# Kernel optimization log

Hardware: AMD Instinct MI355X
Metric: run time of the kernel (lower is better)

The kernel has to match this reference:

```python
import jax, jax.numpy as jnp
import numpy as np

B, N, D = 4, 2048, 512
H, DH = 8, 64  # heads, dim_head; hidden = H*DH = 512


def setup_inputs() -> dict:
    key = jax.random.key(0)
    k1, k2, k3, k4 = jax.random.split(key, 4)
    x = jax.random.normal(k1, (B, N, D), dtype=jnp.float32)
    pos_bias = jax.random.normal(k2, (H, N, N), dtype=jnp.float32) * 0.02
    w_qkv = jax.random.normal(k3, (D, 3 * H * DH), dtype=jnp.float32) * 0.02
    w_out = jax.random.normal(k4, (H * DH, D), dtype=jnp.float32) * 0.02
    return {"x": x, "pos_bias": pos_bias, "w_qkv": w_qkv, "w_out": w_out}


def reference(x, pos_bias, w_qkv, w_out):
    scale = DH ** (-0.5)
    qkv = x @ w_qkv                                   # [B, N, 3*H*DH]
    q, k, v = jnp.split(qkv, 3, axis=-1)
    # '... n (h d) -> ... h n d'
    def split_heads(t):
        return t.reshape(B, N, H, DH).transpose(0, 2, 1, 3)  # [B, H, N, DH]
    q, k, v = split_heads(q), split_heads(k), split_heads(v)
    q = q * scale
    sim = jnp.einsum('bhid,bhjd->bhij', q, k)         # [B, H, N, N]
    sim = sim + pos_bias                              # broadcast over batch
    # original subtracts detached row-max then softmax; jax.nn.softmax does
    # the same stable (stop-gradient max-subtract) computation.
    attn = jax.nn.softmax(sim, axis=-1)
    out = jnp.einsum('bhij,bhjd->bhid', attn, v)      # [B, H, N, DH]
    out = out.transpose(0, 2, 1, 3).reshape(B, N, H * DH)
    return out @ w_out                                # [B, N, D]
```

## Files before the change

### kernel.cpp

```cpp
#include <hip/hip_runtime.h>

typedef short bf16x8 __attribute__((ext_vector_type(8)));
typedef float f32x4 __attribute__((ext_vector_type(4)));

#define MFMA16(a, b, c) __builtin_amdgcn_mfma_f32_16x16x32_bf16(a, b, c, 0, 0, 0)

__device__ __forceinline__ short f2bf(float f) {
  unsigned u = __builtin_bit_cast(unsigned, f);
  u += 0x7fffu + ((u >> 16) & 1u);
  return (short)(u >> 16);
}

__device__ __forceinline__ void gload16(const void* g, void* l) {
  __builtin_amdgcn_global_load_lds(
      (const __attribute__((address_space(1))) void*)g,
      (__attribute__((address_space(3))) void*)l, 16, 0, 0);
}

#define L2E 1.44269504088896f


__global__ __launch_bounds__(256) void cvt_bf16(const float* __restrict__ in,
                                                short* __restrict__ out) {
  size_t i = ((size_t)blockIdx.x * 256 + threadIdx.x) * 8;
  const float4* p = (const float4*)(in + i);
  float4 a = p[0], b = p[1];
  bf16x8 v;
  v[0] = f2bf(a.x); v[1] = f2bf(a.y); v[2] = f2bf(a.z); v[3] = f2bf(a.w);
  v[4] = f2bf(b.x); v[5] = f2bf(b.y); v[6] = f2bf(b.z); v[7] = f2bf(b.w);
  *(bf16x8*)(out + i) = v;
}

__global__ __launch_bounds__(256) void transpose_cvt(const float* __restrict__ in,
                                                     short* __restrict__ out,
                                                     int K, int N) {
  __shared__ short Ts[64][72];
  const int t = threadIdx.x;
  const int k0 = blockIdx.y * 64, n1 = blockIdx.x * 64;
  const int kk = t >> 2, nq = (t & 3) * 16;
  const float* src = in + (size_t)(k0 + kk) * N + n1 + nq;
#pragma unroll
  for (int i = 0; i < 16; ++i) Ts[nq + i][kk] = f2bf(src[i]);
  __syncthreads();
  const int n = t >> 2, kq = (t & 3) * 16;
  short* dst = out + (size_t)(n1 + n) * K + k0 + kq;
  *(bf16x8*)dst = *(const bf16x8*)&Ts[n][kq];
  *(bf16x8*)(dst + 8) = *(const bf16x8*)&Ts[n][kq + 8];
}


__device__ __forceinline__ void gemm128_mainloop(const short* __restrict__ A,
                                                 const short* __restrict__ BT,
                                                 int m0, int n0,
                                                 short (*As)[40], short (*Bs)[40],
                                                 f32x4 acc[4][4]) {
  const int t = threadIdx.x;
  const int w = t >> 6, lane = t & 63, l15 = lane & 15, quad = lane >> 4;
  const int wm = (w & 1) * 64, wn = (w >> 1) * 64;
  const int srow = t >> 1, skg = (t & 1) * 16;
  const short* aptr = A + (size_t)(m0 + srow) * 512 + skg;
  const short* bptr = BT + (size_t)(n0 + srow) * 512 + skg;
  for (int k0 = 0; k0 < 512; k0 += 32) {
    __syncthreads();
    *(bf16x8*)&As[srow][skg]     = *(const bf16x8*)(aptr + k0);
    *(bf16x8*)&As[srow][skg + 8] = *(const bf16x8*)(aptr + k0 + 8);
    *(bf16x8*)&Bs[srow][skg]     = *(const bf16x8*)(bptr + k0);
    *(bf16x8*)&Bs[srow][skg + 8] = *(const bf16x8*)(bptr + k0 + 8);
    __syncthreads();
    bf16x8 af[4], bfr[4];
#pragma unroll
    for (int i = 0; i < 4; ++i) af[i] = *(const bf16x8*)&As[wm + i * 16 + l15][quad * 8];
#pragma unroll
    for (int j = 0; j < 4; ++j) bfr[j] = *(const bf16x8*)&Bs[wn + j * 16 + l15][quad * 8];
#pragma unroll
    for (int i = 0; i < 4; ++i)
#pragma unroll
      for (int j = 0; j < 4; ++j)
        acc[i][j] = MFMA16(af[i], bfr[j], acc[i][j]);
  }
}


__global__ __launch_bounds__(256) void gemm_qkv(const short* __restrict__ A,
                                                const short* __restrict__ BT,
                                                short* __restrict__ q_ws,
                                                short* __restrict__ k_ws,
                                                short* __restrict__ v_t) {
  __shared__ short As[128][40];
  __shared__ short Bs[128][40];
  __shared__ short Ts[64][136];
  const int t = threadIdx.x;
  const int w = t >> 6, lane = t & 63, l15 = lane & 15, quad = lane >> 4;
  const int wm = (w & 1) * 64, wn = (w >> 1) * 64;
  const int m0 = blockIdx.y * 128, n0 = blockIdx.x * 128;
  f32x4 acc[4][4];
#pragma unroll
  for (int i = 0; i < 4; ++i)
#pragma unroll
    for (int j = 0; j < 4; ++j) acc[i][j] = (f32x4){0.f, 0.f, 0.f, 0.f};

  gemm128_mainloop(A, BT, m0, n0, As, Bs, acc);

  const int which = n0 >> 9;
  const int b = m0 >> 11, seq0 = m0 & 2047;
  if (which < 2) {
    short* dst = (which == 0) ? q_ws : k_ws;
    const float scale = (which == 0) ? (0.125f * L2E) : 1.0f;
#pragma unroll
    for (int i = 0; i < 4; ++i)
#pragma unroll
      for (int j = 0; j < 4; ++j)
#pragma unroll
        for (int r = 0; r < 4; ++r) {
          int m_loc = wm + i * 16 + quad * 4 + r;
          int col = n0 + wn + j * 16 + l15;
          int h = (col >> 6) & 7, d = col & 63;
          dst[((size_t)(b * 8 + h) * 2048 + seq0 + m_loc) * 64 + d] =
              f2bf(acc[i][j][r] * scale);
        }
  } else {
    for (int half = 0; half < 2; ++half) {
      __syncthreads();
      if ((w >> 1) == half) {
#pragma unroll
        for (int i = 0; i < 4; ++i)
#pragma unroll
          for (int j = 0; j < 4; ++j)
#pragma unroll
            for (int r = 0; r < 4; ++r)
              Ts[j * 16 + l15][wm + i * 16 + quad * 4 + r] = f2bf(acc[i][j][r]);
      }
      __syncthreads();
      const int hd = ((n0 + half * 64) >> 6) & 7;
      const int dp = t >> 2, sq = (t & 3) * 32;
      short* dstp = v_t + ((size_t)(b * 8 + hd) * 64 + dp) * 2048 + seq0 + sq;
#pragma unroll
      for (int u = 0; u < 4; ++u)
        *(bf16x8*)(dstp + u * 8) = *(const bf16x8*)&Ts[dp][sq + u * 8];
    }
  }
}


#define ATTN_STAGE(BUFD, J0N)                                                  \
  do {                                                                         \
    _Pragma("unroll") for (int i_ = 0; i_ < 2; ++i_) {                         \
      const int ch_ = w * 2 + i_;                                              \
      const int off_ = ch_ * 1024 + lane * 16;                                 \
      const int row_ = off_ >> 7;                                              \
      const int col_ = (off_ & 127) ^ ((row_ & 7) << 4);                       \
      const char* gk_ = (const char*)k_ws +                                    \
          ((size_t)bh * 2048 + (size_t)(J0N) + row_) * 128 + col_;             \
      const char* gv_ = (const char*)v_t +                                     \
          ((size_t)bh * 64 + row_) * 4096 + (size_t)(J0N) * 2 + col_;          \
      gload16(gk_, (char*)&Ks[BUFD][0][0] + ch_ * 1024);                       \
      gload16(gv_, (char*)&Vs[BUFD][0][0] + ch_ * 1024);                       \
    }                                                                          \
  } while (0)

#define ATTN_LOADB(BV, J0N)                                                    \
  do {                                                                         \
    _Pragma("unroll") for (int nt_ = 0; nt_ < 4; ++nt_)                        \
        _Pragma("unroll") for (int r_ = 0; r_ < 4; ++r_)                       \
            BV[nt_][r_] = brow[r_][(J0N) + nt_ * 16];                          \
  } while (0)

#define ATTN_BODY(BUFC, BVC, BVN, J0N, DONEXT)                                 \
  do {                                                                         \
    if (DONEXT) {                                                              \
      ATTN_STAGE((BUFC) ^ 1, (J0N));                                           \
      ATTN_LOADB(BVN, (J0N));                                                  \
    }                                                                          \
    f32x4 S_[4];                                                               \
    _Pragma("unroll") for (int nt_ = 0; nt_ < 4; ++nt_) {                      \
      const char* kb_ = (const char*)&Ks[BUFC][0][0] + (nt_ * 16 + l15) * 128; \
      bf16x8 k0_ = *(const bf16x8*)(kb_ + cs);                                 \
      bf16x8 k1_ = *(const bf16x8*)(kb_ + (cs ^ 64));                          \
      f32x4 s_ = (f32x4){0.f, 0.f, 0.f, 0.f};                                  \
      s_ = MFMA16(aQ0, k0_, s_);                                               \
      s_ = MFMA16(aQ1, k1_, s_);                                               \
      S_[nt_] = s_;                                                            \
    }                                                                          \
    _Pragma("unroll") for (int nt_ = 0; nt_ < 4; ++nt_) {                      \
      float p0_ = exp2f(fmaf(BVC[nt_][0], L2E, S_[nt_][0]));                   \
      float p1_ = exp2f(fmaf(BVC[nt_][1], L2E, S_[nt_][1]));                   \
      float p2_ = exp2f(fmaf(BVC[nt_][2], L2E, S_[nt_][2]));                   \
      float p3_ = exp2f(fmaf(BVC[nt_][3], L2E, S_[nt_][3]));                   \
      lsum[0] += p0_; lsum[1] += p1_; lsum[2] += p2_; lsum[3] += p3_;          \
      unsigned pk01_, pk23_;                                                   \
      asm("v_cvt_pk_bf16_f32 %0, %1, %2" : "=v"(pk01_) : "v"(p0_), "v"(p1_)); \
      asm("v_cvt_pk_bf16_f32 %0, %1, %2" : "=v"(pk23_) : "v"(p2_), "v"(p3_)); \
      char* pb_ = (char*)&Pw[w][0][0];                                         \
      const int c0_ = 2 * (nt_ * 16 + l15);                                    \
      const int q4_ = quad * 4;                                                \
      *(short*)(pb_ + (q4_ + 0) * 128 + (c0_ ^ (((q4_ + 0) & 7) << 4))) =      \
          (short)pk01_;                                                        \
      *(short*)(pb_ + (q4_ + 1) * 128 + (c0_ ^ (((q4_ + 1) & 7) << 4))) =      \
          (short)(pk01_ >> 16);                                                \
      *(short*)(pb_ + (q4_ + 2) * 128 + (c0_ ^ (((q4_ + 2) & 7) << 4))) =      \
          (short)pk23_;                                                        \
      *(short*)(pb_ + (q4_ + 3) * 128 + (c0_ ^ (((q4_ + 3) & 7) << 4))) =      \
          (short)(pk23_ >> 16);                                                \
    }                                                                          \
    {                                                                          \
      const char* pr_ = (const char*)&Pw[w][0][0] + l15 * 128;                 \
      bf16x8 aP0 = *(const bf16x8*)(pr_ + cs);                                 \
      bf16x8 aP1 = *(const bf16x8*)(pr_ + (cs ^ 64));                          \
      _Pragma("unroll") for (int dt_ = 0; dt_ < 4; ++dt_) {                    \
        const char* vb_ =                                                      \
            (const char*)&Vs[BUFC][0][0] + (dt_ * 16 + l15) * 128;             \
        bf16x8 v0_ = *(const bf16x8*)(vb_ + cs);                               \
        bf16x8 v1_ = *(const bf16x8*)(vb_ + (cs ^ 64));                        \
        O[dt_] = MFMA16(aP0, v0_, O[dt_]);                                     \
        O[dt_] = MFMA16(aP1, v1_, O[dt_]);                                     \
      }                                                                        \
    }                                                                          \
    __syncthreads();                                                           \
  } while (0)

__global__ __launch_bounds__(256, 4) void attn_kernel(const short* __restrict__ q_ws,
                                                      const short* __restrict__ k_ws,
                                                      const short* __restrict__ v_t,
                                                      const float* __restrict__ bias,
                                                      short* __restrict__ attnO) {
  __shared__ short Ks[2][64][64];
  __shared__ short Vs[2][64][64];
  __shared__ short Pw[4][16][64];
  const int t = threadIdx.x;
  const int w = t >> 6, lane = t & 63, l15 = lane & 15, quad = lane >> 4;
  const int bid = blockIdx.x;
  const int h = bid & 7;
  const int b = (bid >> 3) & 3;
  const int qb = bid >> 5;
  const int bh = b * 8 + h;
  const int q0 = qb * 64 + w * 16;
  const int cs = (quad * 16) ^ ((l15 & 7) << 4);

  const size_t qbase = ((size_t)bh * 2048 + q0 + l15) * 64 + quad * 8;
  bf16x8 aQ0 = *(const bf16x8*)(q_ws + qbase);
  bf16x8 aQ1 = *(const bf16x8*)(q_ws + qbase + 32);

  f32x4 O[4];
#pragma unroll
  for (int i = 0; i < 4; ++i) O[i] = (f32x4){0.f, 0.f, 0.f, 0.f};
  float lsum[4] = {0.f, 0.f, 0.f, 0.f};

  const float* brow[4];
#pragma unroll
  for (int r = 0; r < 4; ++r)
    brow[r] = bias + ((size_t)h * 2048 + q0 + quad * 4 + r) * 2048 + l15;

  float bvA[4][4], bvB[4][4];
  ATTN_STAGE(0, 0);
  ATTN_LOADB(bvA, 0);
  __syncthreads();

  for (int it = 0; it < 16; ++it) {
    const int j0 = it * 128;
    ATTN_BODY(0, bvA, bvB, j0 + 64, 1);
    ATTN_BODY(1, bvB, bvA, j0 + 128, (it < 15));
  }

#pragma unroll
  for (int off = 1; off <= 8; off <<= 1)
#pragma unroll
    for (int r = 0; r < 4; ++r) lsum[r] += __shfl_xor(lsum[r], off);
#pragma unroll
  for (int r = 0; r < 4; ++r) lsum[r] = 1.f / lsum[r];
#pragma unroll
  for (int dt = 0; dt < 4; ++dt)
#pragma unroll
    for (int r = 0; r < 4; ++r) {
      size_t row = (size_t)b * 2048 + q0 + quad * 4 + r;
      attnO[row * 512 + h * 64 + dt * 16 + l15] = f2bf(O[dt][r] * lsum[r]);
    }
#undef ATTN_STAGE
#undef ATTN_LOADB
#undef ATTN_BODY
}


__global__ __launch_bounds__(256) void gemm_out(const short* __restrict__ A,
                                                const short* __restrict__ BT,
                                                float* __restrict__ out) {
  __shared__ short As[128][40];
  __shared__ short Bs[128][40];
  const int t = threadIdx.x;
  const int w = t >> 6, lane = t & 63, l15 = lane & 15, quad = lane >> 4;
  const int wm = (w & 1) * 64, wn = (w >> 1) * 64;
  const int m0 = blockIdx.y * 128, n0 = blockIdx.x * 128;
  f32x4 acc[4][4];
#pragma unroll
  for (int i = 0; i < 4; ++i)
#pragma unroll
    for (int j = 0; j < 4; ++j) acc[i][j] = (f32x4){0.f, 0.f, 0.f, 0.f};

  gemm128_mainloop(A, BT, m0, n0, As, Bs, acc);

#pragma unroll
  for (int i = 0; i < 4; ++i)
#pragma unroll
    for (int j = 0; j < 4; ++j)
#pragma unroll
      for (int r = 0; r < 4; ++r)
        out[(size_t)(m0 + wm + i * 16 + quad * 4 + r) * 512 + n0 + wn + j * 16 + l15] =
            acc[i][j][r];
}


extern "C" void kernel_launch(void* const* d_in, const int* in_sizes, int n_in,
                              void* d_out, int out_size, void* d_ws, size_t ws_size,
                              hipStream_t stream) {
  (void)in_sizes; (void)n_in; (void)out_size; (void)ws_size;
  const float* x        = (const float*)d_in[0];
  const float* pos_bias = (const float*)d_in[1];
  const float* w_qkv    = (const float*)d_in[2];
  const float* w_out    = (const float*)d_in[3];
  float* out = (float*)d_out;

  short* ws = (short*)d_ws;
  const size_t SEG = (size_t)32 * 2048 * 64;
  short* q_ws  = ws;
  short* k_ws  = q_ws + SEG;
  short* v_t   = k_ws + SEG;
  short* attnO = v_t + SEG;
  short* xbf   = attnO + SEG;
  short* wqkvT = xbf + SEG;
  short* woutT = wqkvT + (size_t)1536 * 512;

  cvt_bf16<<<2048, 256, 0, stream>>>(x, xbf);
  transpose_cvt<<<dim3(24, 8), 256, 0, stream>>>(w_qkv, wqkvT, 512, 1536);
  transpose_cvt<<<dim3(8, 8), 256, 0, stream>>>(w_out, woutT, 512, 512);
  gemm_qkv<<<dim3(12, 64), 256, 0, stream>>>(xbf, wqkvT, q_ws, k_ws, v_t);
  attn_kernel<<<1024, 256, 0, stream>>>(q_ws, k_ws, v_t, pos_bias, attnO);
  gemm_out<<<dim3(4, 64), 256, 0, stream>>>(attnO, woutT, out);
}
```

Before: 374.5 us.

## Double-buffer GEMM mainloop with async global-to-LDS loads and XOR swizzle

Replaces the synchronous register-staged GEMM mainloop used by the QKV and output projections with a double-buffered loop. Tiles are fetched by global_load_lds directly into shared memory, and the next K-slab is prefetched while MFMAs run on the current one. An XOR swizzle replaces the padded LDS layout to avoid bank conflicts, and each iteration now needs one barrier instead of two. The aim is to hide global-load latency in the projection GEMMs, which are a minority of the total time next to attention.

```diff
diff --git a/kernel.cpp b/kernel.cpp
--- a/kernel.cpp
+++ b/kernel.cpp
@@ -49,35 +49,52 @@
 }
 
 
-__device__ __forceinline__ void gemm128_mainloop(const short* __restrict__ A,
-                                                 const short* __restrict__ BT,
-                                                 int m0, int n0,
-                                                 short (*As)[40], short (*Bs)[40],
-                                                 f32x4 acc[4][4]) {
+__device__ __forceinline__ void gemm128_async(const short* __restrict__ A,
+                                              const short* __restrict__ BT,
+                                              int m0, int n0,
+                                              char* As, char* Bs,
+                                              f32x4 acc[4][4]) {
   const int t = threadIdx.x;
   const int w = t >> 6, lane = t & 63, l15 = lane & 15, quad = lane >> 4;
   const int wm = (w & 1) * 64, wn = (w >> 1) * 64;
-  const int srow = t >> 1, skg = (t & 1) * 16;
-  const short* aptr = A + (size_t)(m0 + srow) * 512 + skg;
-  const short* bptr = BT + (size_t)(n0 + srow) * 512 + skg;
-  for (int k0 = 0; k0 < 512; k0 += 32) {
-    __syncthreads();
-    *(bf16x8*)&As[srow][skg]     = *(const bf16x8*)(aptr + k0);
-    *(bf16x8*)&As[srow][skg + 8] = *(const bf16x8*)(aptr + k0 + 8);
-    *(bf16x8*)&Bs[srow][skg]     = *(const bf16x8*)(bptr + k0);
-    *(bf16x8*)&Bs[srow][skg + 8] = *(const bf16x8*)(bptr + k0 + 8);
-    __syncthreads();
+  const int scol = ((lane & 3) ^ ((lane >> 3) & 3)) << 4;
+  const char* ag = (const char*)A + (size_t)(m0 + w * 32 + (lane >> 2)) * 1024 + scol;
+  const char* bg = (const char*)BT + (size_t)(n0 + w * 32 + (lane >> 2)) * 1024 + scol;
+  char* al = As + w * 2048;
+  char* bl = Bs + w * 2048;
+  const int rsw = (quad ^ ((l15 >> 1) & 3)) << 4;
+  const int ra = (wm + l15) * 64 + rsw;
+  const int rb = (wn + l15) * 64 + rsw;
+
+#define GQ_STAGE(BUF, KB)                                                      \
+  do {                                                                         \
+    gload16(ag + (KB), al + (BUF) * 8192);                                     \
+    gload16(ag + 16384 + (KB), al + (BUF) * 8192 + 1024);                      \
+    gload16(bg + (KB), bl + (BUF) * 8192);                                     \
+    gload16(bg + 16384 + (KB), bl + (BUF) * 8192 + 1024);                      \
+  } while (0)
+
+  GQ_STAGE(0, 0);
+  __syncthreads();
+#pragma unroll 2
+  for (int s = 0; s < 16; ++s) {
+    const int buf = s & 1;
+    if (s < 15) GQ_STAGE(buf ^ 1, (s + 1) * 64);
     bf16x8 af[4], bfr[4];
 #pragma unroll
-    for (int i = 0; i < 4; ++i) af[i] = *(const bf16x8*)&As[wm + i * 16 + l15][quad * 8];
-#pragma unroll
-    for (int j = 0; j < 4; ++j) bfr[j] = *(const bf16x8*)&Bs[wn + j * 16 + l15][quad * 8];
+    for (int i = 0; i < 4; ++i)
+      af[i] = *(const bf16x8*)(As + buf * 8192 + ra + i * 1024);
+#pragma unroll
+    for (int j = 0; j < 4; ++j)
+      bfr[j] = *(const bf16x8*)(Bs + buf * 8192 + rb + j * 1024);
 #pragma unroll
     for (int i = 0; i < 4; ++i)
 #pragma unroll
       for (int j = 0; j < 4; ++j)
         acc[i][j] = MFMA16(af[i], bfr[j], acc[i][j]);
+    __syncthreads();
   }
+#undef GQ_STAGE
 }
 
 
@@ -86,8 +103,8 @@
                                                 short* __restrict__ q_ws,
                                                 short* __restrict__ k_ws,
                                                 short* __restrict__ v_t) {
-  __shared__ short As[128][40];
-  __shared__ short Bs[128][40];
+  __shared__ short As[2][128][32];
+  __shared__ short Bs[2][128][32];
   __shared__ short Ts[64][136];
   const int t = threadIdx.x;
   const int w = t >> 6, lane = t & 63, l15 = lane & 15, quad = lane >> 4;
@@ -99,7 +116,7 @@
 #pragma unroll
     for (int j = 0; j < 4; ++j) acc[i][j] = (f32x4){0.f, 0.f, 0.f, 0.f};
 
-  gemm128_mainloop(A, BT, m0, n0, As, Bs, acc);
+  gemm128_async(A, BT, m0, n0, (char*)&As[0][0][0], (char*)&Bs[0][0][0], acc);
 
   const int which = n0 >> 9;
   const int b = m0 >> 11, seq0 = m0 & 2047;
@@ -283,8 +300,8 @@
 __global__ __launch_bounds__(256) void gemm_out(const short* __restrict__ A,
                                                 const short* __restrict__ BT,
                                                 float* __restrict__ out) {
-  __shared__ short As[128][40];
-  __shared__ short Bs[128][40];
+  __shared__ short As[2][128][32];
+  __shared__ short Bs[2][128][32];
   const int t = threadIdx.x;
   const int w = t >> 6, lane = t & 63, l15 = lane & 15, quad = lane >> 4;
   const int wm = (w & 1) * 64, wn = (w >> 1) * 64;
@@ -295,7 +312,7 @@
 #pragma unroll
     for (int j = 0; j < 4; ++j) acc[i][j] = (f32x4){0.f, 0.f, 0.f, 0.f};
 
-  gemm128_mainloop(A, BT, m0, n0, As, Bs, acc);
+  gemm128_async(A, BT, m0, n0, (char*)&As[0][0][0], (char*)&Bs[0][0][0], acc);
 
 #pragma unroll
   for (int i = 0; i < 4; ++i)
```

Result: no change. 368.9 us (-1.5%).
